# Kernel tuning notes

Measured on AMD Instinct MI355X. Metric: run time of the kernel, lower is better.

Reference implementation:

```python
import jax, jax.numpy as jnp
import numpy as np

N_NODES = 50000
N_EDGES = 600000
EMB_DIM = 128
NUM_LAYERS = 5
NUM_ELEM = 118
NUM_CHIR = 4
NUM_BOND_TYPE = 4
NUM_BOND_DIR = 3
BN_EPS = 1e-5


def _xavier(key, shape):
    fan_in, fan_out = shape[0], shape[1]
    limit = np.sqrt(6.0 / (fan_in + fan_out))
    return jax.random.uniform(key, shape, jnp.float32, -limit, limit)


def setup_inputs() -> dict:
    key = jax.random.key(0)
    ks = jax.random.split(key, 12)
    x = jax.random.randint(ks[0], (N_NODES, 2), 0, 4, dtype=jnp.int64)
    edge_index = jax.random.randint(ks[1], (2, N_EDGES), 0, N_NODES, dtype=jnp.int64)
    edge_attr = jax.random.randint(ks[2], (N_EDGES, 2), 0, 3, dtype=jnp.int64)
    elem_emb = _xavier(ks[3], (NUM_ELEM, EMB_DIM))
    chir_emb = _xavier(ks[4], (NUM_CHIR, EMB_DIM))
    bond_type_emb = _xavier(ks[5], (NUM_BOND_TYPE, EMB_DIM))
    bond_dir_emb = _xavier(ks[6], (NUM_BOND_DIR, EMB_DIM))
    # shared GINEConv MLP: Linear(D, 2D) -> ReLU -> Linear(2D, D)
    W1 = _xavier(ks[7], (EMB_DIM, 2 * EMB_DIM))
    b1 = jnp.zeros((2 * EMB_DIM,), jnp.float32)
    W2 = _xavier(ks[8], (2 * EMB_DIM, EMB_DIM))
    b2 = jnp.zeros((EMB_DIM,), jnp.float32)
    # per-layer BatchNorm affine params
    bn_gamma = jnp.ones((NUM_LAYERS, EMB_DIM), jnp.float32)
    bn_beta = jnp.zeros((NUM_LAYERS, EMB_DIM), jnp.float32)
    return {
        "x": x, "edge_index": edge_index, "edge_attr": edge_attr,
        "elem_emb": elem_emb, "chir_emb": chir_emb,
        "bond_type_emb": bond_type_emb, "bond_dir_emb": bond_dir_emb,
        "W1": W1, "b1": b1, "W2": W2, "b2": b2,
        "bn_gamma": bn_gamma, "bn_beta": bn_beta,
    }


def reference(x, edge_index, edge_attr, elem_emb, chir_emb,
              bond_type_emb, bond_dir_emb, W1, b1, W2, b2,
              bn_gamma, bn_beta):
    # input embeddings
    h = elem_emb[x[:, 0]] + chir_emb[x[:, 1]]                    # [N, D]
    e = bond_type_emb[edge_attr[:, 0]] + bond_dir_emb[edge_attr[:, 1]]  # [E, D]
    src, dst = edge_index[0], edge_index[1]
    n = h.shape[0]
    num_layers = bn_gamma.shape[0]
    for layer in range(num_layers):  # conv weights shared across layers
        # GINEConv: msg = relu(x_j + edge_attr), scatter-add, eps=0
        msg = jax.nn.relu(h[src] + e)                            # [E, D]
        agg = jax.ops.segment_sum(msg, dst, num_segments=n)      # [N, D]
        z = h + agg
        out = jax.nn.relu(z @ W1 + b1) @ W2 + b2                 # [N, D]
        # BatchNorm1d (training mode: batch stats, biased variance)
        mean = out.mean(axis=0)
        var = out.var(axis=0)
        out = (out - mean) * jax.lax.rsqrt(var + BN_EPS) * bn_gamma[layer] + bn_beta[layer]
        h = out if layer == num_layers - 1 else jax.nn.relu(out)
    return h
```

## Files before the change

### kernel.cpp

```cpp
#include <hip/hip_runtime.h>

typedef _Float16 f16;
typedef _Float16 f16x8 __attribute__((ext_vector_type(8)));
typedef float f32x4 __attribute__((ext_vector_type(4)));
typedef unsigned short u16;
typedef unsigned int u32;

__device__ __forceinline__ float bf2f(u16 b) {
  union { u32 u; float f; } t; t.u = ((u32)b) << 16; return t.f;
}
__device__ __forceinline__ u16 f2bf(float f) {
  union { float f; u32 u; } t; t.f = f;
  u32 u = t.u;
  return (u16)((u + 0x7FFFu + ((u >> 16) & 1u)) >> 16);
}
__device__ __forceinline__ u16 f2h_bits(float f) {
  f16 h = (f16)f;
  union { f16 h; u16 u; } t; t.h = h; return t.u;
}
__device__ __forceinline__ float2 up2(u32 p) {
  union { u32 u; f16 h[2]; } t; t.u = p;
  float2 r; r.x = (float)t.h[0]; r.y = (float)t.h[1]; return r;
}
__device__ __forceinline__ u32 pk2(float x, float y) {
  return (u32)f2h_bits(x) | ((u32)f2h_bits(y) << 16);
}

__global__ void k_detect(const u16* __restrict__ elemRaw, const int* __restrict__ eiRaw,
                         int* __restrict__ dflags) {
  __shared__ int bad, nzOdd;
  if (threadIdx.x == 0) { bad = 0; nzOdd = 0; }
  __syncthreads();
  int myBad = 0;
  for (int i = threadIdx.x; i < 4096; i += 256) {
    float v = bf2f(elemRaw[i]);
    if (!(v > -0.2f && v < 0.2f)) myBad++;
  }
  if (myBad) atomicAdd(&bad, myBad);
  int myNz = 0;
  for (int i = threadIdx.x; i < 1024; i += 256)
    if (eiRaw[2 * i + 1] != 0) myNz++;
  if (myNz) atomicAdd(&nzOdd, myNz);
  __syncthreads();
  if (threadIdx.x == 0) {
    dflags[0] = (bad == 0) ? 1 : 0;
    dflags[1] = (nzOdd > 16) ? 1 : 0;
  }
}

__global__ void k_init(const u16* __restrict__ elemRaw, const int* __restrict__ eiRaw,
                       int* __restrict__ dflags, int* __restrict__ counts,
                       float* __restrict__ stats, int NPad) {
  if (blockIdx.x == 0) {
    __shared__ int bad, nzOdd;
    if (threadIdx.x == 0) { bad = 0; nzOdd = 0; }
    __syncthreads();
    int myBad = 0;
    for (int i = threadIdx.x; i < 4096; i += 256) {
      float v = bf2f(elemRaw[i]);
      if (!(v > -0.2f && v < 0.2f)) myBad++;
    }
    if (myBad) atomicAdd(&bad, myBad);
    int myNz = 0;
    for (int i = threadIdx.x; i < 1024; i += 256)
      if (eiRaw[2 * i + 1] != 0) myNz++;
    if (myNz) atomicAdd(&nzOdd, myNz);
    __syncthreads();
    if (threadIdx.x == 0) {
      dflags[0] = (bad == 0) ? 1 : 0;
      dflags[1] = (nzOdd > 16) ? 1 : 0;
    }
  } else {
    int i = (blockIdx.x - 1) * 256 + threadIdx.x;
    if (i < NPad) counts[i] = 0;
    else if (i < NPad + 1280) stats[i - NPad] = 0.f;
  }
}

__global__ void k_canary(u32* __restrict__ out, const int* __restrict__ dflags,
                         int out_size, u32 pBf, u32 pF32) {
  int isbf = dflags[0];
  int words = isbf ? (out_size >> 1) : out_size;
  int i = blockIdx.x * 256 + threadIdx.x;
  if (i < words) out[i] = isbf ? pBf : pF32;
}

__global__ void k_cvt(const int* __restrict__ xR, const int* __restrict__ eiR,
                      const int* __restrict__ eaR,
                      const u16* e0, const u16* e1, const u16* e2, const u16* e3,
                      const u16* e4, const u16* e5, const u16* e6, const u16* e7,
                      const u16* e8, const u16* e9,
                      const int* __restrict__ dflags,
                      int* __restrict__ x32, int* __restrict__ ei32, int* __restrict__ combo,
                      int* __restrict__ counts, float* __restrict__ dst,
                      int N, int E, int intBlocks) {
  if ((int)blockIdx.x < intBlocks) {
    int pi = blockIdx.x * 256 + threadIdx.x;
    int nPairs = N + 2 * E;
    if (pi >= nPairs) return;
    int is32 = dflags[1];
    const int* src; int local; int kind;
    if (pi < N) { src = xR; local = pi; kind = 0; }
    else if (pi < N + E) { src = eiR; local = pi - N; kind = 1; }
    else { src = eaR; local = pi - N - E; kind = 2; }
    int j0 = 2 * local;
    int v0, v1;
    if (is32) { int2 v = *(const int2*)(src + j0); v0 = v.x; v1 = v.y; }
    else      { int4 v = *(const int4*)(src + 2 * j0); v0 = v.x; v1 = v.z; }
    if (kind == 0) { x32[j0] = v0; x32[j0 + 1] = v1; }
    else if (kind == 1) {
      ei32[j0] = v0; ei32[j0 + 1] = v1;
      if (j0 >= E) {
        atomicAdd(&counts[v0], 1);
        atomicAdd(&counts[v1], 1);
      }
    } else {
      combo[local] = v0 * 3 + v1;
    }
  } else {
    int i = (blockIdx.x - intBlocks) * 256 + threadIdx.x;
    if (i >= 83712) return;
    int isbf = dflags[0];
    const u16* src; int j;
    if      (i < 15104) { src = e0; j = i; }
    else if (i < 15616) { src = e1; j = i - 15104; }
    else if (i < 16128) { src = e2; j = i - 15616; }
    else if (i < 16512) { src = e3; j = i - 16128; }
    else if (i < 49280) { src = e4; j = i - 16512; }
    else if (i < 49536) { src = e5; j = i - 49280; }
    else if (i < 82304) { src = e6; j = i - 49536; }
    else if (i < 82432) { src = e7; j = i - 82304; }
    else if (i < 83072) { src = e8; j = i - 82432; }
    else                { src = e9; j = i - 83072; }
    dst[i] = isbf ? bf2f(src[j]) : ((const float*)src)[j];
  }
}

__global__ void k_chunksum(const int* __restrict__ counts, int* __restrict__ bsum) {
  int tid = threadIdx.x, lane = tid & 63, w = tid >> 6;
  const int4* c4 = (const int4*)(counts + blockIdx.x * 1024);
  int4 v = c4[tid];
  int s = v.x + v.y + v.z + v.w;
#pragma unroll
  for (int d = 1; d < 64; d <<= 1) s += __shfl_xor(s, d);
  __shared__ int ws[4];
  if (lane == 0) ws[w] = s;
  __syncthreads();
  if (tid == 0) bsum[blockIdx.x] = ws[0] + ws[1] + ws[2] + ws[3];
}

__global__ void k_chunkscan(const int* __restrict__ bsum, int* __restrict__ boff,
                            int* __restrict__ row_start, int N, int nCh) {
  int t = threadIdx.x;
  int v = (t < nCh) ? bsum[t] : 0;
  int incl = v;
#pragma unroll
  for (int d = 1; d < 64; d <<= 1) { int tmp = __shfl_up(incl, d); if (t >= d) incl += tmp; }
  boff[t] = incl - v;
  if (t == 63) row_start[N] = incl;
}

__global__ void k_scanapply(const int* __restrict__ counts, const int* __restrict__ boff,
                            int* __restrict__ row_start, int* __restrict__ cursor, int N) {
  int tid = threadIdx.x, lane = tid & 63, w = tid >> 6;
  int base = blockIdx.x * 1024 + tid * 4;
  int4 v = *(const int4*)(counts + base);
  int tsum = v.x + v.y + v.z + v.w;
  int incl = tsum;
#pragma unroll
  for (int d = 1; d < 64; d <<= 1) { int tmp = __shfl_up(incl, d); if (lane >= d) incl += tmp; }
  __shared__ int ws[4];
  if (lane == 63) ws[w] = incl;
  __syncthreads();
  int woff = 0;
  for (int j = 0; j < w; ++j) woff += ws[j];
  int excl = boff[blockIdx.x] + woff + incl - tsum;
  int e0 = excl, e1 = excl + v.x, e2 = e1 + v.y, e3 = e2 + v.z;
  if (base < N)     { row_start[base] = e0;     cursor[base] = e0; }
  if (base + 1 < N) { row_start[base + 1] = e1; cursor[base + 1] = e1; }
  if (base + 2 < N) { row_start[base + 2] = e2; cursor[base + 2] = e2; }
  if (base + 3 < N) { row_start[base + 3] = e3; cursor[base + 3] = e3; }
}

__global__ void k_scatter(const int* __restrict__ ei, const int* __restrict__ combo,
                          int* cursor, int* packed, int E) {
  int e = blockIdx.x * blockDim.x + threadIdx.x;
  if (e >= E) return;
  int s = ei[e], d = ei[E + e];
  int cb = combo[e];
  int pos = atomicAdd(&cursor[d], 1);
  packed[pos] = s | (cb << 20);
}

__global__ void k_prep(const float* __restrict__ cflt, const int* __restrict__ x,
                       u32* __restrict__ W1F, u32* __restrict__ W2F,
                       u32* __restrict__ tblC, u32* __restrict__ hb, int N, int wtBlocks) {
  if ((int)blockIdx.x < wtBlocks) {
    const float* W1 = cflt + 16512;
    const float* W2 = cflt + 49536;
    const float* bt = cflt + 15616;
    const float* bd = cflt + 16128;
    int g = blockIdx.x * 256 + threadIdx.x;
    {
      int e = g >> 2, wd = g & 3;
      int lane = e & 63, nt = (e >> 6) & 3, ks = (e >> 8) & 3, c = (e >> 10) & 3;
      int q = lane >> 4, lo = lane & 15;
      int n = c * 64 + nt * 16 + lo;
      int k0 = (ks * 4 + q) * 8 + wd * 2;
      W1F[g] = pk2(W1[k0 * 256 + n], W1[(k0 + 1) * 256 + n]);
    }
    {
      int e = g >> 2, wd = g & 3;
      int lane = e & 63, nt = (e >> 6) & 7, ks2 = (e >> 9) & 1, c = (e >> 10) & 3;
      int q = lane >> 4, lo = lane & 15;
      int n2 = nt * 16 + lo;
      int k20 = c * 64 + (ks2 * 4 + q) * 8 + wd * 2;
      W2F[g] = pk2(W2[k20 * 128 + n2], W2[(k20 + 1) * 128 + n2]);
    }
    if (g < 768) {
      int combo = g >> 6, l = g & 63, c0 = l * 2;
      int a0 = combo / 3, a1 = combo - a0 * 3;
      tblC[g] = pk2(bt[a0 * 128 + c0] + bd[a1 * 128 + c0],
                    bt[a0 * 128 + c0 + 1] + bd[a1 * 128 + c0 + 1]);
    }
  } else {
    const float* elem = cflt;
    const float* chir = cflt + 15104;
    int b = blockIdx.x - wtBlocks;
    int wv = (int)(threadIdx.x >> 6);
    int lane = threadIdx.x & 63;
    int node = b * 4 + wv;
    if (node >= N) return;
    int x0 = x[node * 2], x1 = x[node * 2 + 1];
    int c0 = lane * 2;
    float vx = elem[x0 * 128 + c0] + chir[x1 * 128 + c0];
    float vy = elem[x0 * 128 + c0 + 1] + chir[x1 * 128 + c0 + 1];
    hb[(size_t)node * 64 + lane] = pk2(vx, vy);
  }
}

template <bool BN>
__global__ __launch_bounds__(256) void k_agg(
    const u32* __restrict__ hsrc, const int* __restrict__ row_start,
    const int* __restrict__ packed, const u32* __restrict__ tblC,
    const float* __restrict__ statsL, const float* __restrict__ gamma,
    const float* __restrict__ beta, float invN,
    u32* __restrict__ z, int N) {
  __shared__ u32 tbl[768];
  __shared__ float ssc[128], ssh[128];
  for (int idx = threadIdx.x; idx < 768; idx += 256) tbl[idx] = tblC[idx];
  if (BN) {
    if (threadIdx.x < 128) {
      int c = threadIdx.x;
      float mean = statsL[c] * invN;
      float var = statsL[128 + c] * invN - mean * mean;
      float inv = rsqrtf(var + 1e-5f);
      float scv = gamma[c] * inv;
      ssc[c] = scv;
      ssh[c] = beta[c] - mean * scv;
    }
  }
  __syncthreads();
  const uint4* tbl4 = (const uint4*)tbl;
  const int tid = threadIdx.x;
  const int w = tid >> 6, lane = tid & 63;
  const int sub = lane >> 4, li = lane & 15;
  const int node = blockIdx.x * 16 + w * 4 + sub;
  if (node >= N) return;
  float sc[8], sh[8];
  if (BN) {
#pragma unroll
    for (int j = 0; j < 8; ++j) { sc[j] = ssc[li * 8 + j]; sh[j] = ssh[li * 8 + j]; }
  }
  const uint4* hb4 = (const uint4*)hsrc;
  float ax0, ay0, ax1, ay1, ax2, ay2, ax3, ay3;
  {
    uint4 sv = hb4[(size_t)node * 16 + li];
    float2 s0 = up2(sv.x), s1 = up2(sv.y), s2 = up2(sv.z), s3 = up2(sv.w);
    if (BN) {
      s0.x = fmaxf(fmaf(s0.x, sc[0], sh[0]), 0.f); s0.y = fmaxf(fmaf(s0.y, sc[1], sh[1]), 0.f);
      s1.x = fmaxf(fmaf(s1.x, sc[2], sh[2]), 0.f); s1.y = fmaxf(fmaf(s1.y, sc[3], sh[3]), 0.f);
      s2.x = fmaxf(fmaf(s2.x, sc[4], sh[4]), 0.f); s2.y = fmaxf(fmaf(s2.y, sc[5], sh[5]), 0.f);
      s3.x = fmaxf(fmaf(s3.x, sc[6], sh[6]), 0.f); s3.y = fmaxf(fmaf(s3.y, sc[7], sh[7]), 0.f);
    }
    ax0 = s0.x; ay0 = s0.y; ax1 = s1.x; ay1 = s1.y;
    ax2 = s2.x; ay2 = s2.y; ax3 = s3.x; ay3 = s3.y;
  }
  const int s_ = row_start[node], e_ = row_start[node + 1];
  int p = s_;

#define ACCP(RW, TW, I0, AX, AY)                                       \
  {                                                                    \
    float2 rv = up2(RW); float2 tv = up2(TW);                          \
    float hx, hy;                                                      \
    if (BN) {                                                          \
      hx = fmaxf(fmaf(rv.x, sc[I0], sh[I0]), 0.f);                     \
      hy = fmaxf(fmaf(rv.y, sc[I0 + 1], sh[I0 + 1]), 0.f);             \
    } else { hx = rv.x; hy = rv.y; }                                   \
    AX += fmaxf(hx + tv.x, 0.f);                                       \
    AY += fmaxf(hy + tv.y, 0.f);                                       \
  }

  for (; p + 4 <= e_; p += 4) {
    int k0 = packed[p], k1 = packed[p + 1], k2 = packed[p + 2], k3 = packed[p + 3];
    uint4 r0 = hb4[(size_t)(k0 & 0xFFFFF) * 16 + li];
    uint4 r1 = hb4[(size_t)(k1 & 0xFFFFF) * 16 + li];
    uint4 r2 = hb4[(size_t)(k2 & 0xFFFFF) * 16 + li];
    uint4 r3 = hb4[(size_t)(k3 & 0xFFFFF) * 16 + li];
    uint4 t0 = tbl4[(k0 >> 20) * 16 + li];
    uint4 t1 = tbl4[(k1 >> 20) * 16 + li];
    uint4 t2 = tbl4[(k2 >> 20) * 16 + li];
    uint4 t3 = tbl4[(k3 >> 20) * 16 + li];
    ACCP(r0.x, t0.x, 0, ax0, ay0)
    ACCP(r0.y, t0.y, 2, ax1, ay1)
    ACCP(r0.z, t0.z, 4, ax2, ay2)
    ACCP(r0.w, t0.w, 6, ax3, ay3)
    ACCP(r1.x, t1.x, 0, ax0, ay0)
    ACCP(r1.y, t1.y, 2, ax1, ay1)
    ACCP(r1.z, t1.z, 4, ax2, ay2)
    ACCP(r1.w, t1.w, 6, ax3, ay3)
    ACCP(r2.x, t2.x, 0, ax0, ay0)
    ACCP(r2.y, t2.y, 2, ax1, ay1)
    ACCP(r2.z, t2.z, 4, ax2, ay2)
    ACCP(r2.w, t2.w, 6, ax3, ay3)
    ACCP(r3.x, t3.x, 0, ax0, ay0)
    ACCP(r3.y, t3.y, 2, ax1, ay1)
    ACCP(r3.z, t3.z, 4, ax2, ay2)
    ACCP(r3.w, t3.w, 6, ax3, ay3)
  }
  for (; p < e_; ++p) {
    int k0 = packed[p];
    uint4 r0 = hb4[(size_t)(k0 & 0xFFFFF) * 16 + li];
    uint4 t0 = tbl4[(k0 >> 20) * 16 + li];
    ACCP(r0.x, t0.x, 0, ax0, ay0)
    ACCP(r0.y, t0.y, 2, ax1, ay1)
    ACCP(r0.z, t0.z, 4, ax2, ay2)
    ACCP(r0.w, t0.w, 6, ax3, ay3)
  }
#undef ACCP
  uint4 o;
  o.x = pk2(ax0, ay0); o.y = pk2(ax1, ay1); o.z = pk2(ax2, ay2); o.w = pk2(ax3, ay3);
  ((uint4*)z)[(size_t)node * 16 + li] = o;
}

__global__ __launch_bounds__(512, 2) void k_mlp(
    const u16* __restrict__ z, const u32* __restrict__ W1F, const u32* __restrict__ W2F,
    const float* __restrict__ b1, const float* __restrict__ b2,
    u16* __restrict__ act, float* __restrict__ statsL, int N, int nTiles) {
  __shared__ u32 sW1[16384];
  __shared__ u32 sW2[16384];
  __shared__ u16 sYp[8][1024];
  __shared__ float sStats[256];

  const int tid = threadIdx.x;
  const int w = tid >> 6, lane = tid & 63;
  const int lo = lane & 15, q = lane >> 4;

  if (tid < 256) sStats[tid] = 0.f;
  {
    const int4* gW1 = (const int4*)W1F;
    const int4* gW2 = (const int4*)W2F;
    int4* lW1 = (int4*)sW1;
    int4* lW2 = (int4*)sW2;
#pragma unroll
    for (int it = 0; it < 8; ++it) {
      int o = it * 512 + tid;
      lW1[o] = gW1[o];
      lW2[o] = gW2[o];
    }
  }
  __syncthreads();

  float rb1[16], rb2[8];
#pragma unroll
  for (int c = 0; c < 4; ++c)
#pragma unroll
    for (int nt = 0; nt < 4; ++nt)
      rb1[c * 4 + nt] = b1[c * 64 + nt * 16 + lo];
#pragma unroll
  for (int nt = 0; nt < 8; ++nt)
    rb2[nt] = b2[nt * 16 + lo];

  float aSum[8] = {}, aSq[8] = {};
  u16* myY = sYp[w];

  for (int t = blockIdx.x * 8 + w; t < nTiles; t += 2048) {
    const int row0 = t * 16;
    f16x8 a1[4];
    const char* zrow = (const char*)z + (size_t)(row0 + lo) * 256;
#pragma unroll
    for (int ks = 0; ks < 4; ++ks)
      a1[ks] = *(const f16x8*)(zrow + (ks * 4 + q) * 16);

    f32x4 accO[8] = {};
#pragma unroll
    for (int c = 0; c < 4; ++c) {
      f16x8 B1[16];
#pragma unroll
      for (int i = 0; i < 16; ++i)
        B1[i] = *(const f16x8*)((const char*)sW1 + ((c * 16 + i) << 10) + lane * 16);
      f32x4 acc1[4] = {};
#pragma unroll
      for (int ks = 0; ks < 4; ++ks)
#pragma unroll
        for (int nt = 0; nt < 4; ++nt)
          acc1[nt] = __builtin_amdgcn_mfma_f32_16x16x32_f16(a1[ks], B1[ks * 4 + nt], acc1[nt], 0, 0, 0);
#pragma unroll
      for (int nt = 0; nt < 4; ++nt) {
        int ycol = nt * 16 + lo;
        float bias = rb1[c * 4 + nt];
#pragma unroll
        for (int i = 0; i < 4; ++i) {
          int m = q * 4 + i;
          float v = fmaxf(acc1[nt][i] + bias, 0.f);
          myY[m * 64 + (((ycol >> 3) ^ (m & 7)) << 3) + (ycol & 7)] = f2h_bits(v);
        }
      }
      f16x8 B2[16];
#pragma unroll
      for (int i = 0; i < 16; ++i)
        B2[i] = *(const f16x8*)((const char*)sW2 + ((c * 16 + i) << 10) + lane * 16);
#pragma unroll
      for (int ks2 = 0; ks2 < 2; ++ks2) {
        int kq2 = ks2 * 4 + q;
        f16x8 a2 = *(const f16x8*)(myY + lo * 64 + ((kq2 ^ (lo & 7)) << 3));
#pragma unroll
        for (int nt = 0; nt < 8; ++nt)
          accO[nt] = __builtin_amdgcn_mfma_f32_16x16x32_f16(a2, B2[ks2 * 8 + nt], accO[nt], 0, 0, 0);
      }
    }
#pragma unroll
    for (int nt = 0; nt < 8; ++nt) {
      int n2 = nt * 16 + lo;
      float bias = rb2[nt];
#pragma unroll
      for (int i = 0; i < 4; ++i) {
        int row = row0 + q * 4 + i;
        float v = accO[nt][i] + bias;
        act[(size_t)row * 128 + n2] = f2h_bits(v);
        if (row < N) { aSum[nt] += v; aSq[nt] += v * v; }
      }
    }
  }

#pragma unroll
  for (int nt = 0; nt < 8; ++nt) {
    float s = aSum[nt], s2 = aSq[nt];
    s += __shfl_xor(s, 16); s += __shfl_xor(s, 32);
    s2 += __shfl_xor(s2, 16); s2 += __shfl_xor(s2, 32);
    if (q == 0) {
      atomicAdd(&sStats[nt * 16 + lo], s);
      atomicAdd(&sStats[128 + nt * 16 + lo], s2);
    }
  }
  __syncthreads();
  if (tid < 256) atomicAdd(&statsL[tid], sStats[tid]);
}

__global__ __launch_bounds__(256) void k_final(
    const u32* __restrict__ act, const float* __restrict__ statsL,
    const float* __restrict__ gamma, const float* __restrict__ beta,
    float invN, const int* __restrict__ dflags, void* __restrict__ outv, int N) {
  __shared__ float ssc[128], ssh[128];
  int tid = threadIdx.x;
  if (tid < 128) {
    float mean = statsL[tid] * invN;
    float var = statsL[128 + tid] * invN - mean * mean;
    float inv = rsqrtf(var + 1e-5f);
    float scv = gamma[tid] * inv;
    ssc[tid] = scv;
    ssh[tid] = beta[tid] - mean * scv;
  }
  __syncthreads();
  int isbf = dflags[0];
  int total = N * 64;
  for (int i = blockIdx.x * 256 + tid; i < total; i += gridDim.x * 256) {
    int c0 = (i & 63) * 2;
    float2 v = up2(act[i]);
    float ox = v.x * ssc[c0] + ssh[c0];
    float oy = v.y * ssc[c0 + 1] + ssh[c0 + 1];
    if (isbf) ((u32*)outv)[i] = (u32)f2bf(ox) | ((u32)f2bf(oy) << 16);
    else { float2 o; o.x = ox; o.y = oy; ((float2*)outv)[i] = o; }
  }
}

extern "C" void kernel_launch(void* const* d_in, const int* in_sizes, int n_in,
                              void* d_out, int out_size, void* d_ws, size_t ws_size,
                              hipStream_t stream) {
  const int* xR  = (const int*)d_in[0];
  const int* eiR = (const int*)d_in[1];
  const int* eaR = (const int*)d_in[2];
  const u16* emR = (const u16*)d_in[3];
  const u16* chR = (const u16*)d_in[4];
  const u16* btR = (const u16*)d_in[5];
  const u16* bdR = (const u16*)d_in[6];
  const u16* W1R = (const u16*)d_in[7];
  const u16* b1R = (const u16*)d_in[8];
  const u16* W2R = (const u16*)d_in[9];
  const u16* b2R = (const u16*)d_in[10];
  const u16* gR  = (const u16*)d_in[11];
  const u16* beR = (const u16*)d_in[12];

  const int N = in_sizes[0] / 2;
  const int E = in_sizes[1] / 2;
  const int L = in_sizes[11] / 128;
  const int Mpad = ((N + 63) / 64) * 64;
  const int nCh = (N + 1023) / 1024;
  const int NPad = nCh * 1024;
  const int nTiles = (N + 15) / 16;

  char* base = (char*)d_ws;
  size_t off = 0;
  auto take = [&](size_t bytes) -> void* {
    void* p = base + off;
    off += (bytes + 255) & ~(size_t)255;
    return p;
  };
  int*   dflags    = (int*)  take(256);
  int*   x32       = (int*)  take((size_t)2 * N * 4);
  int*   ei32      = (int*)  take((size_t)2 * E * 4);
  int*   combo     = (int*)  take((size_t)E * 4);
  float* cflt      = (float*)take(83712 * 4);
  u32*   act       = (u32*)  take((size_t)Mpad * 64 * 4);
  u32*   hb        = (u32*)  take((size_t)Mpad * 64 * 4);
  u16*   zb        = (u16*)  take((size_t)Mpad * 128 * 2);
  int*   packed    = (int*)  take((size_t)E * 4);
  int*   row_start = (int*)  take((size_t)(N + 1) * 4);
  int*   cursor    = (int*)  take((size_t)N * 4);
  int*   counts    = (int*)  take((size_t)NPad * 4);
  int*   bsum      = (int*)  take(64 * 4);
  int*   boff      = (int*)  take(64 * 4);
  float* stats     = (float*)take((size_t)L * 256 * 4);
  u32*   W1F       = (u32*)  take(16384 * 4);
  u32*   W2F       = (u32*)  take(16384 * 4);
  u32*   tblC      = (u32*)  take(768 * 4);
  const size_t need = off;
  (void)n_in;

  float* cB1 = cflt + 49280;
  float* cB2 = cflt + 82304;
  float* cGamma = cflt + 82432;
  float* cBeta = cflt + 83072;

  if (need > ws_size) {
    k_detect<<<dim3(1), dim3(256), 0, stream>>>(emR, eiR, dflags);
    k_canary<<<dim3((out_size + 255) / 256), dim3(256), 0, stream>>>(
        (u32*)d_out, dflags, out_size, 0x40004000u, 0x40000000u);
    return;
  }

  const int nzBlocks = (NPad + 1280 + 255) / 256;
  k_init<<<dim3(nzBlocks + 1), dim3(256), 0, stream>>>(emR, eiR, dflags, counts, stats, NPad);

  const int nPairs = N + 2 * E;
  const int intBlocks = (nPairs + 255) / 256;
  const int fltBlocks = (83712 + 255) / 256;
  k_cvt<<<dim3(intBlocks + fltBlocks), dim3(256), 0, stream>>>(
      xR, eiR, eaR, emR, chR, btR, bdR, W1R, b1R, W2R, b2R, gR, beR,
      dflags, x32, ei32, combo, counts, cflt, N, E, intBlocks);

  k_chunksum<<<dim3(nCh), dim3(256), 0, stream>>>(counts, bsum);
  k_chunkscan<<<dim3(1), dim3(64), 0, stream>>>(bsum, boff, row_start, N, nCh);
  k_scanapply<<<dim3(nCh), dim3(256), 0, stream>>>(counts, boff, row_start, cursor, N);
  k_scatter<<<dim3((E + 255) / 256), dim3(256), 0, stream>>>(ei32, combo, cursor, packed, E);

  const int wtBlocks = 64;
  k_prep<<<dim3(wtBlocks + (N + 3) / 4), dim3(256), 0, stream>>>(
      cflt, x32, W1F, W2F, tblC, hb, N, wtBlocks);

  const float invN = 1.0f / (float)N;
  for (int l = 0; l < L; ++l) {
    if (l == 0) {
      k_agg<false><<<dim3((N + 15) / 16), dim3(256), 0, stream>>>(
          hb, row_start, packed, tblC, nullptr, nullptr, nullptr, 0.f, (u32*)zb, N);
    } else {
      k_agg<true><<<dim3((N + 15) / 16), dim3(256), 0, stream>>>(
          act, row_start, packed, tblC, stats + (size_t)(l - 1) * 256,
          cGamma + (size_t)(l - 1) * 128, cBeta + (size_t)(l - 1) * 128, invN,
          (u32*)zb, N);
    }
    k_mlp<<<dim3(256), dim3(512), 0, stream>>>(
        zb, W1F, W2F, cB1, cB2, (u16*)act, stats + (size_t)l * 256, N, nTiles);
  }
  k_final<<<dim3(1024), dim3(256), 0, stream>>>(
      act, stats + (size_t)(L - 1) * 256, cGamma + (size_t)(L - 1) * 128,
      cBeta + (size_t)(L - 1) * 128, invN, dflags, d_out, N);
}
```

Before: 460.1 us.

## Use one wavefront per node in aggregation and widen MLP blocks to twelve waves

New measurement: 568.4 us. 1.24x slower.

```diff
diff --git a/kernel.cpp b/kernel.cpp
--- a/kernel.cpp
+++ b/kernel.cpp
@@ -249,142 +249,96 @@
   __shared__ u32 tbl[768];
   __shared__ float ssc[128], ssh[128];
   for (int idx = threadIdx.x; idx < 768; idx += 256) tbl[idx] = tblC[idx];
+  if (BN && threadIdx.x < 128) {
+    int c = threadIdx.x;
+    float mean = statsL[c] * invN;
+    float var = statsL[128 + c] * invN - mean * mean;
+    float inv = rsqrtf(var + 1e-5f);
+    float scv = gamma[c] * inv;
+    ssc[c] = scv;
+    ssh[c] = beta[c] - mean * scv;
+  }
+  __syncthreads();
+  const int w = threadIdx.x >> 6, lane = threadIdx.x & 63;
+  const int node = blockIdx.x * 4 + w;
+  if (node >= N) return;
+  float scx, scy, shx, shy;
   if (BN) {
-    if (threadIdx.x < 128) {
-      int c = threadIdx.x;
-      float mean = statsL[c] * invN;
-      float var = statsL[128 + c] * invN - mean * mean;
-      float inv = rsqrtf(var + 1e-5f);
-      float scv = gamma[c] * inv;
-      ssc[c] = scv;
-      ssh[c] = beta[c] - mean * scv;
-    }
-  }
-  __syncthreads();
-  const uint4* tbl4 = (const uint4*)tbl;
-  const int tid = threadIdx.x;
-  const int w = tid >> 6, lane = tid & 63;
-  const int sub = lane >> 4, li = lane & 15;
-  const int node = blockIdx.x * 16 + w * 4 + sub;
-  if (node >= N) return;
-  float sc[8], sh[8];
-  if (BN) {
-#pragma unroll
-    for (int j = 0; j < 8; ++j) { sc[j] = ssc[li * 8 + j]; sh[j] = ssh[li * 8 + j]; }
-  }
-  const uint4* hb4 = (const uint4*)hsrc;
-  float ax0, ay0, ax1, ay1, ax2, ay2, ax3, ay3;
+    scx = ssc[2 * lane]; scy = ssc[2 * lane + 1];
+    shx = ssh[2 * lane]; shy = ssh[2 * lane + 1];
+  }
+  float ax, ay;
   {
-    uint4 sv = hb4[(size_t)node * 16 + li];
-    float2 s0 = up2(sv.x), s1 = up2(sv.y), s2 = up2(sv.z), s3 = up2(sv.w);
+    float2 sv = up2(hsrc[(size_t)node * 64 + lane]);
     if (BN) {
-      s0.x = fmaxf(fmaf(s0.x, sc[0], sh[0]), 0.f); s0.y = fmaxf(fmaf(s0.y, sc[1], sh[1]), 0.f);
-      s1.x = fmaxf(fmaf(s1.x, sc[2], sh[2]), 0.f); s1.y = fmaxf(fmaf(s1.y, sc[3], sh[3]), 0.f);
-      s2.x = fmaxf(fmaf(s2.x, sc[4], sh[4]), 0.f); s2.y = fmaxf(fmaf(s2.y, sc[5], sh[5]), 0.f);
-      s3.x = fmaxf(fmaf(s3.x, sc[6], sh[6]), 0.f); s3.y = fmaxf(fmaf(s3.y, sc[7], sh[7]), 0.f);
-    }
-    ax0 = s0.x; ay0 = s0.y; ax1 = s1.x; ay1 = s1.y;
-    ax2 = s2.x; ay2 = s2.y; ax3 = s3.x; ay3 = s3.y;
+      sv.x = fmaxf(fmaf(sv.x, scx, shx), 0.f);
+      sv.y = fmaxf(fmaf(sv.y, scy, shy), 0.f);
+    }
+    ax = sv.x; ay = sv.y;
   }
   const int s_ = row_start[node], e_ = row_start[node + 1];
-  int p = s_;
-
-#define ACCP(RW, TW, I0, AX, AY)                                       \
-  {                                                                    \
-    float2 rv = up2(RW); float2 tv = up2(TW);                          \
-    float hx, hy;                                                      \
-    if (BN) {                                                          \
-      hx = fmaxf(fmaf(rv.x, sc[I0], sh[I0]), 0.f);                     \
-      hy = fmaxf(fmaf(rv.y, sc[I0 + 1], sh[I0 + 1]), 0.f);             \
-    } else { hx = rv.x; hy = rv.y; }                                   \
-    AX += fmaxf(hx + tv.x, 0.f);                                       \
-    AY += fmaxf(hy + tv.y, 0.f);                                       \
-  }
-
-  for (; p + 4 <= e_; p += 4) {
-    int k0 = packed[p], k1 = packed[p + 1], k2 = packed[p + 2], k3 = packed[p + 3];
-    uint4 r0 = hb4[(size_t)(k0 & 0xFFFFF) * 16 + li];
-    uint4 r1 = hb4[(size_t)(k1 & 0xFFFFF) * 16 + li];
-    uint4 r2 = hb4[(size_t)(k2 & 0xFFFFF) * 16 + li];
-    uint4 r3 = hb4[(size_t)(k3 & 0xFFFFF) * 16 + li];
-    uint4 t0 = tbl4[(k0 >> 20) * 16 + li];
-    uint4 t1 = tbl4[(k1 >> 20) * 16 + li];
-    uint4 t2 = tbl4[(k2 >> 20) * 16 + li];
-    uint4 t3 = tbl4[(k3 >> 20) * 16 + li];
-    ACCP(r0.x, t0.x, 0, ax0, ay0)
-    ACCP(r0.y, t0.y, 2, ax1, ay1)
-    ACCP(r0.z, t0.z, 4, ax2, ay2)
-    ACCP(r0.w, t0.w, 6, ax3, ay3)
-    ACCP(r1.x, t1.x, 0, ax0, ay0)
-    ACCP(r1.y, t1.y, 2, ax1, ay1)
-    ACCP(r1.z, t1.z, 4, ax2, ay2)
-    ACCP(r1.w, t1.w, 6, ax3, ay3)
-    ACCP(r2.x, t2.x, 0, ax0, ay0)
-    ACCP(r2.y, t2.y, 2, ax1, ay1)
-    ACCP(r2.z, t2.z, 4, ax2, ay2)
-    ACCP(r2.w, t2.w, 6, ax3, ay3)
-    ACCP(r3.x, t3.x, 0, ax0, ay0)
-    ACCP(r3.y, t3.y, 2, ax1, ay1)
-    ACCP(r3.z, t3.z, 4, ax2, ay2)
-    ACCP(r3.w, t3.w, 6, ax3, ay3)
-  }
-  for (; p < e_; ++p) {
-    int k0 = packed[p];
-    uint4 r0 = hb4[(size_t)(k0 & 0xFFFFF) * 16 + li];
-    uint4 t0 = tbl4[(k0 >> 20) * 16 + li];
-    ACCP(r0.x, t0.x, 0, ax0, ay0)
-    ACCP(r0.y, t0.y, 2, ax1, ay1)
-    ACCP(r0.z, t0.z, 4, ax2, ay2)
-    ACCP(r0.w, t0.w, 6, ax3, ay3)
-  }
-#undef ACCP
-  uint4 o;
-  o.x = pk2(ax0, ay0); o.y = pk2(ax1, ay1); o.z = pk2(ax2, ay2); o.w = pk2(ax3, ay3);
-  ((uint4*)z)[(size_t)node * 16 + li] = o;
-}
-
-__global__ __launch_bounds__(512, 2) void k_mlp(
+  for (int p = s_; p < e_; p += 8) {
+    int kk[8]; u32 rr[8], tt[8];
+#pragma unroll
+    for (int j = 0; j < 8; ++j)
+      kk[j] = packed[(p + j < e_) ? (p + j) : (e_ - 1)];
+#pragma unroll
+    for (int j = 0; j < 8; ++j)
+      rr[j] = hsrc[(size_t)(kk[j] & 0xFFFFF) * 64 + lane];
+#pragma unroll
+    for (int j = 0; j < 8; ++j)
+      tt[j] = tbl[(kk[j] >> 20) * 64 + lane];
+#pragma unroll
+    for (int j = 0; j < 8; ++j) {
+      if (p + j < e_) {
+        float2 rv = up2(rr[j]);
+        float2 tv = up2(tt[j]);
+        float hx, hy;
+        if (BN) {
+          hx = fmaxf(fmaf(rv.x, scx, shx), 0.f);
+          hy = fmaxf(fmaf(rv.y, scy, shy), 0.f);
+        } else { hx = rv.x; hy = rv.y; }
+        ax += fmaxf(hx + tv.x, 0.f);
+        ay += fmaxf(hy + tv.y, 0.f);
+      }
+    }
+  }
+  z[(size_t)node * 64 + lane] = pk2(ax, ay);
+}
+
+__global__ __launch_bounds__(768, 1) void k_mlp(
     const u16* __restrict__ z, const u32* __restrict__ W1F, const u32* __restrict__ W2F,
     const float* __restrict__ b1, const float* __restrict__ b2,
     u16* __restrict__ act, float* __restrict__ statsL, int N, int nTiles) {
   __shared__ u32 sW1[16384];
   __shared__ u32 sW2[16384];
-  __shared__ u16 sYp[8][1024];
+  __shared__ u16 sYp[12][1024];
   __shared__ float sStats[256];
+  __shared__ float sB1[256];
+  __shared__ float sB2[128];
 
   const int tid = threadIdx.x;
   const int w = tid >> 6, lane = tid & 63;
   const int lo = lane & 15, q = lane >> 4;
 
-  if (tid < 256) sStats[tid] = 0.f;
+  if (tid < 256) { sStats[tid] = 0.f; sB1[tid] = b1[tid]; }
+  if (tid < 128) sB2[tid] = b2[tid];
   {
     const int4* gW1 = (const int4*)W1F;
     const int4* gW2 = (const int4*)W2F;
     int4* lW1 = (int4*)sW1;
     int4* lW2 = (int4*)sW2;
-#pragma unroll
-    for (int it = 0; it < 8; ++it) {
-      int o = it * 512 + tid;
+    for (int o = tid; o < 4096; o += 768) {
       lW1[o] = gW1[o];
       lW2[o] = gW2[o];
     }
   }
   __syncthreads();
 
-  float rb1[16], rb2[8];
-#pragma unroll
-  for (int c = 0; c < 4; ++c)
-#pragma unroll
-    for (int nt = 0; nt < 4; ++nt)
-      rb1[c * 4 + nt] = b1[c * 64 + nt * 16 + lo];
-#pragma unroll
-  for (int nt = 0; nt < 8; ++nt)
-    rb2[nt] = b2[nt * 16 + lo];
-
   float aSum[8] = {}, aSq[8] = {};
   u16* myY = sYp[w];
 
-  for (int t = blockIdx.x * 8 + w; t < nTiles; t += 2048) {
+  for (int t = blockIdx.x * 12 + w; t < nTiles; t += 3072) {
     const int row0 = t * 16;
     f16x8 a1[4];
     const char* zrow = (const char*)z + (size_t)(row0 + lo) * 256;
@@ -408,7 +362,7 @@
 #pragma unroll
       for (int nt = 0; nt < 4; ++nt) {
         int ycol = nt * 16 + lo;
-        float bias = rb1[c * 4 + nt];
+        float bias = sB1[c * 64 + nt * 16 + lo];
 #pragma unroll
         for (int i = 0; i < 4; ++i) {
           int m = q * 4 + i;
@@ -432,7 +386,7 @@
 #pragma unroll
     for (int nt = 0; nt < 8; ++nt) {
       int n2 = nt * 16 + lo;
-      float bias = rb2[nt];
+      float bias = sB2[nt * 16 + lo];
 #pragma unroll
       for (int i = 0; i < 4; ++i) {
         int row = row0 + q * 4 + i;
@@ -571,15 +525,15 @@
   const float invN = 1.0f / (float)N;
   for (int l = 0; l < L; ++l) {
     if (l == 0) {
-      k_agg<false><<<dim3((N + 15) / 16), dim3(256), 0, stream>>>(
+      k_agg<false><<<dim3((N + 3) / 4), dim3(256), 0, stream>>>(
           hb, row_start, packed, tblC, nullptr, nullptr, nullptr, 0.f, (u32*)zb, N);
     } else {
-      k_agg<true><<<dim3((N + 15) / 16), dim3(256), 0, stream>>>(
+      k_agg<true><<<dim3((N + 3) / 4), dim3(256), 0, stream>>>(
           act, row_start, packed, tblC, stats + (size_t)(l - 1) * 256,
           cGamma + (size_t)(l - 1) * 128, cBeta + (size_t)(l - 1) * 128, invN,
           (u32*)zb, N);
     }
-    k_mlp<<<dim3(256), dim3(512), 0, stream>>>(
+    k_mlp<<<dim3(256), dim3(768), 0, stream>>>(
         zb, W1F, W2F, cB1, cB2, (u16*)act, stats + (size_t)l * 256, N, nTiles);
   }
   k_final<<<dim3(1024), dim3(256), 0, stream>>>(
```
